# Kernel tuning notes

Measured on AMD Instinct MI355X. Metric: run time of the kernel, lower is better.

Reference implementation:

```python
import jax, jax.numpy as jnp
import numpy as np
from jax import lax

NEG = -1e9


def cyk(scores, lens):
    """Inside algorithm (logsumexp semiring) for a span tree-CRF.
    scores: [B, N, N]; scores[b, i, j] = potential of right-closed span [i, j].
    lens:   [B] int sentence lengths.
    Returns logZ[b] = inside score of span [0, lens[b]-1].
    Chart A[b, i, w] = inside score of span starting at i with width w.
    Recurrence: A[i, w] = D[i, w] + logsumexp_{u=1..w-1}(A[i, u] + A[i+u, w-u]).
    """
    B, N = scores.shape[0], scores.shape[1]
    i = jnp.arange(N)
    u = jnp.arange(N + 1)
    # D[b, i, w] = scores[b, i, i+w-1] (span of width w starting at i)
    j_end = jnp.clip(i[:, None] + u[None, :] - 1, 0, N - 1)          # [N, N+1]
    D = jnp.take_along_axis(scores, j_end[None], axis=2)             # [B, N, N+1]
    valid_span = (u[None, :] >= 1) & (i[:, None] + u[None, :] <= N)  # [N, N+1]
    D = jnp.where(valid_span[None], D, NEG)

    A = jnp.full((B, N, N + 1), NEG, scores.dtype)
    A = A.at[:, :, 1].set(D[:, :, 1])  # width-1 spans
    rowc = jnp.clip(i[:, None] + u[None, :], 0, N - 1)               # [N, N+1]

    def step(A, w):
        colc = jnp.broadcast_to(jnp.clip(w - u, 0, N), (N, N + 1))
        right = A[:, rowc, colc]                                     # A[b, i+u, w-u]
        ok = (u[None, :] >= 1) & (u[None, :] <= w - 1) & (i[:, None] + u[None, :] <= N - 1)
        tmp = jnp.where(ok[None], A + right, NEG)                    # splits over u
        new = jax.nn.logsumexp(tmp, axis=-1) + D[:, :, w]
        return A.at[:, :, w].set(new), None

    A, _ = lax.scan(step, A, jnp.arange(2, N + 1))
    return jnp.take_along_axis(A[:, 0, :], lens[:, None], axis=1)[:, 0]


def setup_inputs() -> dict:
    key = jax.random.key(0)
    k1, k2 = jax.random.split(key)
    B, N = 64, 256
    span_logits = jax.random.normal(k1, (B, N, N, 2), jnp.float32)
    spans_ind = jax.random.randint(k2, (B, N, N), 0, 3).astype(jnp.int32)
    maskspan = jnp.ones((B, N, N), bool)
    span_mask = jnp.zeros((B, N, N), bool)
    return {"span_logits": span_logits, "spans_ind": spans_ind,
            "maskspan": maskspan, "span_mask": span_mask}


def reference(span_logits, spans_ind, maskspan, span_mask):
    # spans_ind: values>0 shifted down by 1, then to bool (gold span indicator)
    sind = jnp.where(spans_ind > 0, spans_ind - 1, spans_ind).astype(bool)
    # hard masking path (smoothing == 1.0, norm == False, ent_lamb == 0.0)
    s0 = jnp.where(span_mask | sind, NEG, span_logits[..., 0])
    s1 = jnp.where(span_mask | ~sind, NEG, span_logits[..., 1])
    ob = jnp.logaddexp(s0, s1)                                  # gold-constrained potentials
    allv = jnp.logaddexp(span_logits[..., 0], span_logits[..., 1])  # unconstrained
    lens = maskspan[:, 0].sum(-1).astype(jnp.int32)
    marginals = cyk(ob, lens)
    logz = cyk(allv, lens)
    return (logz - marginals).sum() / maskspan[:, 0].sum().astype(span_logits.dtype)
```

## Files before the change

### kernel.cpp

```cpp
#include <hip/hip_runtime.h>


#define NN 256
#define BATCH 64
#define NCHART (2 * BATCH)
#define NEGV -1000000000.0f
#define NEGB -1.0e30f
#define K2f 1.4426950408889634f
#define LN2f 0.6931471805599453f

#define CHARTF 32896
#define CMAXF 260
#define BB_OFF (CHARTF + CMAXF)
#define FLG_OFF (BB_OFF + 16)
#define SCR_OFF (FLG_OFF + 260)
#define SCRF 3952
#define LDSF (SCR_OFF + SCRF)

#define RES_OFF ((size_t)16)
#define LEN_OFF ((size_t)(16 + NCHART))
#define FB_OFF  ((size_t)(16 + NCHART + BATCH + 16))

__device__ __forceinline__ float fexp2(float x) {
#if __has_builtin(__builtin_amdgcn_exp2f)
    return __builtin_amdgcn_exp2f(x);
#else
    return exp2f(x);
#endif
}

__device__ __forceinline__ float wave_max64(float x) {
    int v = __float_as_int(x);
    int s;
    s = __builtin_amdgcn_update_dpp(v, v, 0x111, 0xf, 0xf, false);
    v = __float_as_int(fmaxf(__int_as_float(v), __int_as_float(s)));
    s = __builtin_amdgcn_update_dpp(v, v, 0x112, 0xf, 0xf, false);
    v = __float_as_int(fmaxf(__int_as_float(v), __int_as_float(s)));
    s = __builtin_amdgcn_update_dpp(v, v, 0x114, 0xf, 0xf, false);
    v = __float_as_int(fmaxf(__int_as_float(v), __int_as_float(s)));
    s = __builtin_amdgcn_update_dpp(v, v, 0x118, 0xf, 0xf, false);
    v = __float_as_int(fmaxf(__int_as_float(v), __int_as_float(s)));
    s = __builtin_amdgcn_update_dpp(v, v, 0x142, 0xa, 0xf, false);
    v = __float_as_int(fmaxf(__int_as_float(v), __int_as_float(s)));
    s = __builtin_amdgcn_update_dpp(v, v, 0x143, 0xc, 0xf, false);
    v = __float_as_int(fmaxf(__int_as_float(v), __int_as_float(s)));
    return __int_as_float(__builtin_amdgcn_readlane(v, 63));
}

__device__ __forceinline__ float rlane(float v, int idx) {
    return __int_as_float(__builtin_amdgcn_readlane(__float_as_int(v), idx));
}

__device__ __forceinline__ int cstart(int v) {
    return 257 * (v - 1) - ((v * (v - 1)) >> 1);
}

__device__ __forceinline__ float score_at(const float* __restrict__ logits,
                                          const int* __restrict__ spans_ind,
                                          const void* __restrict__ span_mask,
                                          int isb, int t, int b, int i, int j) {
    size_t sidx = ((size_t)b * NN + i) * NN + j;
    float l0 = logits[2 * sidx];
    float l1 = logits[2 * sidx + 1];
    if (t) {
        float mx = fmaxf(l0, l1), mn = fminf(l0, l1);
        return mx + log1pf(__expf(mn - mx));
    } else {
        bool sind = (spans_ind[sidx] == 2);
        bool sm = isb ? (((const unsigned char*)span_mask)[sidx] != 0)
                      : (((const int*)span_mask)[sidx] != 0);
        float s0 = (sm || sind)  ? NEGV : l0;
        float s1 = (sm || !sind) ? NEGV : l1;
        float mx = fmaxf(s0, s1), mn = fminf(s0, s1);
        return mx + log1pf(__expf(mn - mx));
    }
}

template <int KK>
__device__ __forceinline__ void group8(
    float* __restrict__ Lc, float* __restrict__ scr, float* __restrict__ cm,
    float* __restrict__ bbuf, int* flg, float* __restrict__ sres,
    int W, int tid, int wave, int lane, int lenv) {
    const int ES = 257 - W;

    {
        const int g = wave >> 1;
        const int half = wave & 1;
        const int L = W + g;
        if (L <= 256) {
            const int E = 257 - L;
            float b = NEGB;
            for (int uu = g + 1 + lane; uu <= W - 1; uu += 64)
                b = fmaxf(b, cm[uu] + cm[L - uu]);
            b = wave_max64(b);
            if (lane == 0 && half == 0) bbuf[g] = b;

            const int n_int = W - 1 - g;
            const int h0 = (n_int + 1) >> 1;
            const int ua = half ? (g + 1 + h0) : (g + 1);
            const int ub = half ? (W - 1) : (g + h0);
            const int R = ub - ua + 1;

            float su0, su1 = 0.f;
            {
                int uu = ua + lane;
                int uc = (uu <= ub) ? uu : ub;
                su0 = fexp2(cm[uc] + cm[L - uc] - b);
                if (R > 64) {
                    int uu2 = ua + 64 + lane;
                    int uc2 = (uu2 <= ub) ? uu2 : ub;
                    su1 = fexp2(cm[uc2] + cm[L - uc2] - b);
                }
            }

            float acc[KK];
#pragma unroll
            for (int k = 0; k < KK; ++k) acc[k] = 0.f;

            if (R > 0) {
                int la = cstart(ua) + lane;
                int ra = cstart(L - ua) + ua + lane;
                int A = 257 - ua, B = 257 - (L - ua);
                const int R0 = (R < 64) ? R : 64;
#pragma unroll 2
                for (int idx = 0; idx < R0; ++idx) {
                    float su = rlane(su0, idx);
#pragma unroll
                    for (int k = 0; k < KK; ++k)
                        acc[k] = fmaf(su * Lc[la + 64 * k],
                                      Lc[ra + 64 * k], acc[k]);
                    la += A; A -= 1;
                    ra -= B; B += 1;
                }
#pragma unroll 2
                for (int idx = 64; idx < R; ++idx) {
                    float su = rlane(su1, idx - 64);
#pragma unroll
                    for (int k = 0; k < KK; ++k)
                        acc[k] = fmaf(su * Lc[la + 64 * k],
                                      Lc[ra + 64 * k], acc[k]);
                    la += A; A -= 1;
                    ra -= B; B += 1;
                }
            }
#pragma unroll
            for (int k = 0; k < KK; ++k) {
                int ge = lane + 64 * k;
                if (ge < E) scr[wave * ES + ge] = acc[k];
            }
        }
    }
    __syncthreads();

    if (wave < 8) {
        const int g = wave;
        const int L = W + g;
        if (L <= 256) {
            const int E = 257 - L;
            float m = bbuf[g];

            float s[KK];
#pragma unroll
            for (int k = 0; k < KK; ++k) {
                int ge = lane + 64 * k;
                s[k] = (ge < E) ? scr[(2 * g) * ES + ge] +
                                  scr[(2 * g + 1) * ES + ge]
                                : 0.f;
            }

            for (int j = g; j >= 1; --j) {
                const int v = L - j;
                while (((volatile int*)flg)[v] == 0) {}
                asm volatile("" ::: "memory");
                float pm = cm[j] + cm[v];
                float nm = fmaxf(m, pm);
                float sc = fexp2(m - nm), pj = fexp2(pm - nm);
                const int cj = cstart(j), cl = cstart(v);
#pragma unroll
                for (int k = 0; k < KK; ++k) {
                    int ge = lane + 64 * k;
                    if (ge < E) {
                        float tt = Lc[cj + ge] * Lc[cl + ge + j] +
                                   Lc[cl + ge] * Lc[cj + ge + v];
                        s[k] = fmaf(s[k], sc, pj * tt);
                    }
                }
                m = nm;
            }

            float xa[KK];
            float mx = NEGB;
#pragma unroll
            for (int k = 0; k < KK; ++k) {
                int ge = lane + 64 * k;
                float av = NEGB;
                if (ge < E) av = Lc[cstart(L) + ge] + m + __log2f(s[k]);
                xa[k] = av;
                mx = fmaxf(mx, av);
            }
            mx = wave_max64(mx);
#pragma unroll
            for (int k = 0; k < KK; ++k) {
                int ge = lane + 64 * k;
                if (ge < E) Lc[cstart(L) + ge] = fexp2(xa[k] - mx);
            }
            if (lane == 0) {
                cm[L] = mx;
                if (L == lenv) *sres = xa[0];
            }
            __threadfence_block();
            asm volatile("" ::: "memory");
            if (lane == 0) ((volatile int*)flg)[L] = 1;
        }
    }
    __syncthreads();
}

__device__ __forceinline__ void level_direct(
    float* __restrict__ Lc, float* __restrict__ cm,
    float* __restrict__ swm, float* __restrict__ sres,
    int w, int tid, int wave, int lane, int lenv) {
    const int E = NN + 1 - w;
    float a = NEGB;
    if (tid < E) {
        float b0 = NEGB;
        for (int u = 1; u <= w - 1; ++u) b0 = fmaxf(b0, cm[u] + cm[w - u]);
        float s = 0.f;
        for (int u = 1; u <= w - 1; ++u) {
            float su = fexp2(cm[u] + cm[w - u] - b0);
            s = fmaf(su * Lc[cstart(u) + tid], Lc[cstart(w - u) + u + tid], s);
        }
        int ad = cstart(w) + tid;
        a = Lc[ad] + b0 + __log2f(s);
        Lc[ad] = a;
        if (tid == 0 && w == lenv) *sres = a;
    }
    float m = wave_max64(a);
    if (lane == 0) swm[wave] = m;
    __syncthreads();
    float cmw = swm[0];
#pragma unroll
    for (int i = 1; i < 16; ++i) cmw = fmaxf(cmw, swm[i]);
    if (tid < E) {
        int ad = cstart(w) + tid;
        Lc[ad] = fexp2(Lc[ad] - cmw);
    }
    if (tid == 0) cm[w] = cmw;
    __syncthreads();
}

template <bool USE_LDS>
__global__ __launch_bounds__(1024) void cyk_kernel(
    const float* __restrict__ logits,
    const int* __restrict__ spans_ind,
    const void* __restrict__ maskspan,
    const void* __restrict__ span_mask,
    float* __restrict__ ws) {
    extern __shared__ float lds[];
    const int c = blockIdx.x;
    const int b = c >> 1;
    const int t = c & 1;
    const int tid = threadIdx.x;
    const int wave = tid >> 6, lane = tid & 63;

    float* __restrict__ Lc = USE_LDS ? lds : (ws + FB_OFF + (size_t)c * LDSF);
    float* __restrict__ cm = Lc + CHARTF;
    float* __restrict__ bbuf = Lc + BB_OFF;
    int* flg = (int*)(Lc + FLG_OFF);
    float* __restrict__ scr = Lc + SCR_OFF;

    __shared__ int s_len;
    __shared__ int s_isb;
    __shared__ float s_wmax[16];
    __shared__ float s_res;
    if (tid == 0) {
        s_len = 0;
        s_res = K2f * NEGV;
        unsigned probe = *(const unsigned*)maskspan;
        s_isb = (probe > 1u) ? 1 : 0;
    }
    if (tid < 260) flg[tid] = 0;
    __syncthreads();
    const int isb = s_isb;

    if (tid < NN) {
        size_t off = (size_t)b * NN * NN + tid;
        int v = isb ? (((const unsigned char*)maskspan)[off] ? 1 : 0)
                    : (((const int*)maskspan)[off] ? 1 : 0);
        atomicAdd(&s_len, v);
    }

    for (int it = 0; it < 64; ++it) {
        int f = (it << 10) + tid;
        int i = f >> 8, j = f & 255;
        if (j >= i) {
            float sc = score_at(logits, spans_ind, span_mask, isb, t, b, i, j);
            Lc[cstart(j - i + 1) + i] = K2f * sc;
        }
    }
    __syncthreads();
    const int lenv = s_len;

    {
        float a = (tid < NN) ? Lc[tid] : NEGB;
        if (tid == 0 && lenv == 1) s_res = a;
        float m = wave_max64(a);
        if (lane == 0) s_wmax[wave] = m;
        __syncthreads();
        float c1 = s_wmax[0];
#pragma unroll
        for (int i = 1; i < 16; ++i) c1 = fmaxf(c1, s_wmax[i]);
        if (tid < NN) Lc[tid] = fexp2(a - c1);
        if (tid == 0) cm[1] = c1;
    }
    __syncthreads();

    for (int w = 2; w <= 9; ++w)
        level_direct(Lc, cm, s_wmax, &s_res, w, tid, wave, lane, lenv);
    for (int W = 10; W <= 58; W += 8)
        group8<4>(Lc, scr, cm, bbuf, flg, &s_res, W, tid, wave, lane, lenv);
    for (int W = 66; W <= 122; W += 8)
        group8<3>(Lc, scr, cm, bbuf, flg, &s_res, W, tid, wave, lane, lenv);
    for (int W = 130; W <= 186; W += 8)
        group8<2>(Lc, scr, cm, bbuf, flg, &s_res, W, tid, wave, lane, lenv);
    for (int W = 194; W <= 250; W += 8)
        group8<1>(Lc, scr, cm, bbuf, flg, &s_res, W, tid, wave, lane, lenv);

    if (tid == 0) {
        int len = s_len;
        float rres = (len >= 1) ? (s_res * LN2f) : NEGV;
        ws[RES_OFF + c] = rres;
        if (t == 0) ws[LEN_OFF + b] = (float)len;
    }
}

__global__ __launch_bounds__(64) void finish_kernel(const float* __restrict__ ws,
                                                    float* __restrict__ out) {
    int b = threadIdx.x;
    float diff = ws[RES_OFF + 2 * b + 1] - ws[RES_OFF + 2 * b];
    float len  = ws[LEN_OFF + b];
    for (int d = 32; d > 0; d >>= 1) {
        diff += __shfl_xor(diff, d);
        len  += __shfl_xor(len, d);
    }
    if (b == 0) out[0] = diff / len;
}

extern "C" void kernel_launch(void* const* d_in, const int* in_sizes, int n_in,
                              void* d_out, int out_size, void* d_ws, size_t ws_size,
                              hipStream_t stream) {
    const float* logits    = (const float*)d_in[0];
    const int*   spans_ind = (const int*)d_in[1];
    const void*  maskspan  = d_in[2];
    const void*  span_mask = d_in[3];
    float* ws = (float*)d_ws;

    const size_t shbytes = (size_t)LDSF * sizeof(float);
    hipError_t e = hipFuncSetAttribute(
        reinterpret_cast<const void*>(&cyk_kernel<true>),
        hipFuncAttributeMaxDynamicSharedMemorySize, (int)shbytes);
    if (e == hipSuccess) {
        hipLaunchKernelGGL(cyk_kernel<true>, dim3(NCHART), dim3(1024), shbytes,
                           stream, logits, spans_ind, maskspan, span_mask, ws);
    } else {
        hipLaunchKernelGGL(cyk_kernel<false>, dim3(NCHART), dim3(1024), 0,
                           stream, logits, spans_ind, maskspan, span_mask, ws);
    }
    hipLaunchKernelGGL(finish_kernel, dim3(1), dim3(64), 0, stream,
                       ws, (float*)d_out);
}
```

Before: 490.1 us.

## Pair adjacent span widths per wave to share left-chart loads across splits

Each group of four waves now computes two adjacent output widths (g0, g1) together, splitting the u range into quarters, so the left-operand chart load is reused for both widths. This is meant to cut LDS reads per FMA and drop the second split loop. In exchange it adds an extra barrier and a two-phase store/accumulate into scratch, computes two max reductions per wave, and assumes R never exceeds 64 per quarter. It also wastes work on invalid lanes for g1.

```diff
diff --git a/kernel.cpp b/kernel.cpp
--- a/kernel.cpp
+++ b/kernel.cpp
@@ -84,69 +84,92 @@
     const int ES = 257 - W;
 
     {
-        const int g = wave >> 1;
-        const int half = wave & 1;
-        const int L = W + g;
-        if (L <= 256) {
-            const int E = 257 - L;
-            float b = NEGB;
-            for (int uu = g + 1 + lane; uu <= W - 1; uu += 64)
-                b = fmaxf(b, cm[uu] + cm[L - uu]);
-            b = wave_max64(b);
-            if (lane == 0 && half == 0) bbuf[g] = b;
-
-            const int n_int = W - 1 - g;
-            const int h0 = (n_int + 1) >> 1;
-            const int ua = half ? (g + 1 + h0) : (g + 1);
-            const int ub = half ? (W - 1) : (g + h0);
-            const int R = ub - ua + 1;
-
-            float su0, su1 = 0.f;
-            {
-                int uu = ua + lane;
-                int uc = (uu <= ub) ? uu : ub;
-                su0 = fexp2(cm[uc] + cm[L - uc] - b);
-                if (R > 64) {
-                    int uu2 = ua + 64 + lane;
-                    int uc2 = (uu2 <= ub) ? uu2 : ub;
-                    su1 = fexp2(cm[uc2] + cm[L - uc2] - b);
+        const int p  = wave >> 2;
+        const int sp = wave & 3;
+        const int g0 = 2 * p, g1 = g0 + 1;
+        const int L0 = W + g0, L1 = W + g1;
+        const bool has1 = (L1 <= 256);
+        const int E0 = 257 - L0;
+        const int E1 = has1 ? (257 - L1) : 0;
+
+        float b0 = NEGB, b1 = NEGB;
+        for (int uu = g0 + 1 + lane; uu <= W - 1; uu += 64)
+            b0 = fmaxf(b0, cm[uu] + cm[L0 - uu]);
+        b0 = wave_max64(b0);
+        if (has1) {
+            for (int uu = g1 + 1 + lane; uu <= W - 1; uu += 64)
+                b1 = fmaxf(b1, cm[uu] + cm[L1 - uu]);
+            b1 = wave_max64(b1);
+        }
+        if (lane == 0 && sp == 0) {
+            bbuf[g0] = b0;
+            if (has1) bbuf[g1] = b1;
+        }
+
+        const int n = W - 1 - g0;
+        const int C = (n + 3) >> 2;
+        const int ua = g0 + 1 + sp * C;
+        const int ub = min(ua + C - 1, W - 1);
+        const int R = ub - ua + 1;
+
+        float su0r, su1r;
+        {
+            int u = ua + lane;
+            int uc = (u <= ub) ? u : ub;
+            bool v0 = (lane < R);
+            bool v1 = v0 && has1 && (uc >= g1 + 1);
+            float e0 = fexp2(cm[uc] + cm[L0 - uc] - b0);
+            float e1 = fexp2(cm[uc] + cm[L1 - uc] - b1);
+            su0r = v0 ? e0 : 0.f;
+            su1r = v1 ? e1 : 0.f;
+        }
+
+        float acc0[KK], acc1[KK];
+#pragma unroll
+        for (int k = 0; k < KK; ++k) { acc0[k] = 0.f; acc1[k] = 0.f; }
+
+        if (R > 0) {
+            int la  = cstart(ua) + lane;
+            int ra0 = cstart(L0 - ua) + ua + lane;
+            int ra1 = cstart(L1 - ua) + ua + lane;
+            int A  = 257 - ua;
+            int B0 = 257 - (L0 - ua);
+            int B1 = 257 - (L1 - ua);
+#pragma unroll 2
+            for (int idx = 0; idx < R; ++idx) {
+                float su0 = rlane(su0r, idx);
+                float su1 = rlane(su1r, idx);
+#pragma unroll
+                for (int k = 0; k < KK; ++k) {
+                    float lv = Lc[la  + 64 * k];
+                    float r0 = Lc[ra0 + 64 * k];
+                    float r1 = Lc[ra1 + 64 * k];
+                    acc0[k] = fmaf(su0 * lv, r0, acc0[k]);
+                    acc1[k] = fmaf(su1 * lv, r1, acc1[k]);
                 }
-            }
-
-            float acc[KK];
-#pragma unroll
-            for (int k = 0; k < KK; ++k) acc[k] = 0.f;
-
-            if (R > 0) {
-                int la = cstart(ua) + lane;
-                int ra = cstart(L - ua) + ua + lane;
-                int A = 257 - ua, B = 257 - (L - ua);
-                const int R0 = (R < 64) ? R : 64;
-#pragma unroll 2
-                for (int idx = 0; idx < R0; ++idx) {
-                    float su = rlane(su0, idx);
-#pragma unroll
-                    for (int k = 0; k < KK; ++k)
-                        acc[k] = fmaf(su * Lc[la + 64 * k],
-                                      Lc[ra + 64 * k], acc[k]);
-                    la += A; A -= 1;
-                    ra -= B; B += 1;
-                }
-#pragma unroll 2
-                for (int idx = 64; idx < R; ++idx) {
-                    float su = rlane(su1, idx - 64);
-#pragma unroll
-                    for (int k = 0; k < KK; ++k)
-                        acc[k] = fmaf(su * Lc[la + 64 * k],
-                                      Lc[ra + 64 * k], acc[k]);
-                    la += A; A -= 1;
-                    ra -= B; B += 1;
-                }
-            }
-#pragma unroll
-            for (int k = 0; k < KK; ++k) {
-                int ge = lane + 64 * k;
-                if (ge < E) scr[wave * ES + ge] = acc[k];
+                la += A; A -= 1;
+                ra0 -= B0; B0 += 1;
+                ra1 -= B1; B1 += 1;
+            }
+        }
+
+        const int s0 = 4 * p + (sp & 1);
+        const int s1 = s0 + 2;
+        if (sp >= 2) {
+#pragma unroll
+            for (int k = 0; k < KK; ++k) {
+                int ge = lane + 64 * k;
+                if (ge < E0) scr[s0 * ES + ge] = acc0[k];
+                if (ge < E1) scr[s1 * ES + ge] = acc1[k];
+            }
+        }
+        __syncthreads();
+        if (sp < 2) {
+#pragma unroll
+            for (int k = 0; k < KK; ++k) {
+                int ge = lane + 64 * k;
+                if (ge < E0) scr[s0 * ES + ge] += acc0[k];
+                if (ge < E1) scr[s1 * ES + ge] += acc1[k];
             }
         }
     }
```

Measured after the change: 476.5 us. -2.8%, faster.
